# Performance work log

Hardware: AMD Instinct MI355X
Metric: run time of the kernel (lower is better)

The kernel has to match this reference:

```python
import jax, jax.numpy as jnp
import numpy as np

N_NODES = 100000
EPS = 1e-12  # F.normalize eps


def _glorot(key, shape):
    fan_in, fan_out = shape[0], shape[1]
    lim = (6.0 / (fan_in + fan_out)) ** 0.5
    return jax.random.uniform(key, shape, jnp.float32, -lim, lim)


def setup_inputs() -> dict:
    key = jax.random.key(0)
    ks = jax.random.split(key, 8)
    d_in, d_hid, d_out = 128, 128, 64
    x = jax.random.normal(ks[0], (N_NODES, d_in), jnp.float32)
    edge_index = jax.random.randint(ks[1], (2, 1600000), 0, N_NODES, jnp.int32)
    return {
        "x": x,
        "edge_index": edge_index,
        "Wl1": _glorot(ks[2], (d_in, d_hid)),
        "Wr1": _glorot(ks[3], (d_in, d_hid)),
        "b1": jnp.zeros((d_hid,), jnp.float32),
        "Wl2": _glorot(ks[4], (d_hid, d_out)),
        "Wr2": _glorot(ks[5], (d_hid, d_out)),
        "b2": jnp.zeros((d_out,), jnp.float32),
    }


def _sage_conv(x, src, dst, Wl, Wr, b):
    # gather source-node features per edge, max-aggregate onto destinations
    msgs = x[src]                                   # [E, d]
    agg = jax.ops.segment_max(msgs, dst, num_segments=N_NODES)
    # PyG scatter-max leaves 0 for nodes with no incoming edges
    agg = jnp.where(jnp.isneginf(agg), 0.0, agg)    # [N, d]
    out = agg @ Wl + x @ Wr + b                     # lin_l(aggr) + lin_r(root)
    # normalize=True -> L2 normalize rows (F.normalize semantics)
    norm = jnp.maximum(jnp.linalg.norm(out, axis=-1, keepdims=True), EPS)
    return out / norm


def reference(x, edge_index, Wl1, Wr1, b1, Wl2, Wr2, b2):
    src, dst = edge_index[0], edge_index[1]
    # dropout p=0.9 is identity in eval mode
    h = jax.nn.relu(_sage_conv(x, src, dst, Wl1, Wr1, b1))
    return _sage_conv(h, src, dst, Wl2, Wr2, b2)
```

## Files before the change

### kernel.cpp

```cpp
#include <hip/hip_runtime.h>
#include <math.h>

typedef __attribute__((ext_vector_type(8))) short short8;
typedef __attribute__((ext_vector_type(4))) float floatx4;

static __device__ __forceinline__ ushort f32_to_bf16_rne(float f) {
  union { float f; unsigned int i; } c;
  c.f = f;
  unsigned int lsb = (c.i >> 16) & 1u;
  c.i += 0x7fffu + lsb;
  return (ushort)(c.i >> 16);
}
static __device__ __forceinline__ float bf16_lo(unsigned int v) {
  union { unsigned int i; float f; } c;
  c.i = v << 16;
  return c.f;
}
static __device__ __forceinline__ float bf16_hi(unsigned int v) {
  union { unsigned int i; float f; } c;
  c.i = v & 0xffff0000u;
  return c.f;
}


#define NBLK 256

__global__ __launch_bounds__(256) void binhist_kernel(const int* __restrict__ dst,
                                                      int* __restrict__ bh, int E, int EBLK,
                                                      int NBUCKET) {
  __shared__ int h[256];
  int t = threadIdx.x, blk = blockIdx.x;
  h[t] = 0;
  __syncthreads();
  int e0 = blk * EBLK, e1 = min(E, e0 + EBLK);
  for (int e = e0 + t; e < e1; e += 256) atomicAdd(&h[dst[e] >> 9], 1);
  __syncthreads();
  if (t < NBUCKET) bh[t * NBLK + blk] = h[t];
}

__global__ void scan1_kernel(const int* __restrict__ counts, int* __restrict__ offsets,
                             int* __restrict__ tileSums, int N) {
  __shared__ int sd[256];
  int t = threadIdx.x;
  int base = blockIdx.x * 1024 + t * 4;
  int v[4];
#pragma unroll
  for (int i = 0; i < 4; i++) v[i] = (base + i < N) ? counts[base + i] : 0;
  int s = v[0] + v[1] + v[2] + v[3];
  sd[t] = s;
  __syncthreads();
  int acc = s;
  for (int off = 1; off < 256; off <<= 1) {
    int add = (t >= off) ? sd[t - off] : 0;
    __syncthreads();
    acc += add;
    sd[t] = acc;
    __syncthreads();
  }
  int run = acc - s;
#pragma unroll
  for (int i = 0; i < 4; i++) {
    if (base + i < N) offsets[base + i] = run;
    run += v[i];
  }
  if (t == 255) tileSums[blockIdx.x] = acc;
}

__global__ void scan2_kernel(int* __restrict__ tileSums, int nT) {
  __shared__ int sd[128];
  int t = threadIdx.x;
  int v = (t < nT) ? tileSums[t] : 0;
  sd[t] = v;
  __syncthreads();
  int acc = v;
  for (int off = 1; off < 128; off <<= 1) {
    int add = (t >= off) ? sd[t - off] : 0;
    __syncthreads();
    acc += add;
    sd[t] = acc;
    __syncthreads();
  }
  if (t < nT) tileSums[t] = acc - v;
}

__global__ void scan3_nc_kernel(int* __restrict__ offsets, const int* __restrict__ tileSums,
                                int N) {
  int i = blockIdx.x * 256 + threadIdx.x;
  if (i >= N) return;
  offsets[i] += tileSums[i >> 10];
}

__global__ __launch_bounds__(256) void binscatter_kernel(const int* __restrict__ src,
                                                         const int* __restrict__ dst,
                                                         const int* __restrict__ bhOff,
                                                         int2* __restrict__ binned, int E,
                                                         int EBLK, int NBUCKET) {
  __shared__ int cur[256];
  int t = threadIdx.x, blk = blockIdx.x;
  if (t < NBUCKET) cur[t] = bhOff[t * NBLK + blk];
  __syncthreads();
  int e0 = blk * EBLK, e1 = min(E, e0 + EBLK);
  for (int e = e0 + t; e < e1; e += 256) {
    int d = dst[e];
    int pos = atomicAdd(&cur[d >> 9], 1);
    binned[pos] = make_int2(src[e], d);
  }
}

__global__ __launch_bounds__(256) void bucket_build_kernel(
    const int2* __restrict__ binned, const int* __restrict__ bhOff, int* __restrict__ counts,
    int* __restrict__ offsets, int* __restrict__ csr, int N, int E, int NBUCKET) {
  __shared__ int h[512];
  __shared__ int lofs[512];
  __shared__ int cur[512];
  __shared__ int sd[256];
  int b = blockIdx.x, t = threadIdx.x;
  int S = bhOff[b * NBLK];
  int Send = (b + 1 < NBUCKET) ? bhOff[(b + 1) * NBLK] : E;
  h[t] = 0;
  h[t + 256] = 0;
  __syncthreads();
  for (int e = S + t; e < Send; e += 256) atomicAdd(&h[binned[e].y & 511], 1);
  __syncthreads();
  int h0 = h[2 * t], h1 = h[2 * t + 1];
  int s = h0 + h1;
  sd[t] = s;
  __syncthreads();
  int acc = s;
  for (int off = 1; off < 256; off <<= 1) {
    int add = (t >= off) ? sd[t - off] : 0;
    __syncthreads();
    acc += add;
    sd[t] = acc;
    __syncthreads();
  }
  int run = acc - s;
  lofs[2 * t] = run;
  lofs[2 * t + 1] = run + h0;
  __syncthreads();
  int node0 = b * 512;
#pragma unroll
  for (int i = 0; i < 2; i++) {
    int l = t + i * 256;
    int node = node0 + l;
    if (node < N) {
      counts[node] = h[l];
      offsets[node] = S + lofs[l];
    }
    cur[l] = S + lofs[l];
  }
  __syncthreads();
  for (int e = S + t; e < Send; e += 256) {
    int2 r = binned[e];
    int pos = atomicAdd(&cur[r.y & 511], 1);
    csr[pos] = r.x;
  }
}


__global__ void f32_to_bf16_kernel(const float* __restrict__ in, ushort* __restrict__ out, int n) {
  int i = (blockIdx.x * 256 + threadIdx.x) * 8;
  if (i >= n) return;
  float4 a = *(const float4*)(in + i);
  float4 b = *(const float4*)(in + i + 4);
  union { ushort u[8]; short8 v; } r;
  r.u[0] = f32_to_bf16_rne(a.x); r.u[1] = f32_to_bf16_rne(a.y);
  r.u[2] = f32_to_bf16_rne(a.z); r.u[3] = f32_to_bf16_rne(a.w);
  r.u[4] = f32_to_bf16_rne(b.x); r.u[5] = f32_to_bf16_rne(b.y);
  r.u[6] = f32_to_bf16_rne(b.z); r.u[7] = f32_to_bf16_rne(b.w);
  *(short8*)(out + i) = r.v;
}

__global__ void wt_conv_kernel(const float* __restrict__ W, ushort* __restrict__ WT, int K, int C) {
  int idx = blockIdx.x * 256 + threadIdx.x;
  if (idx >= K * C) return;
  int k = idx / C, c = idx % C;
  WT[(size_t)c * K + k] = f32_to_bf16_rne(W[idx]);
}


__global__ void agg_max_bf16_kernel(const ushort* __restrict__ feat, const int* __restrict__ csr,
                                    const int* __restrict__ offsets, const int* __restrict__ counts,
                                    unsigned int* __restrict__ aggb, int N) {
  int lane = threadIdx.x & 63;
  int node = (blockIdx.x * blockDim.x + threadIdx.x) >> 6;
  if (node >= N) return;
  const unsigned int* fu = (const unsigned int*)feat;
  int start = offsets[node];
  int deg = counts[node];
  float m0 = 0.0f, m1 = 0.0f;
  if (deg > 0) {
    m0 = -INFINITY;
    m1 = -INFINITY;
    int e = 0;
    for (; e + 4 <= deg; e += 4) {
      int s0 = csr[start + e + 0];
      int s1 = csr[start + e + 1];
      int s2 = csr[start + e + 2];
      int s3 = csr[start + e + 3];
      unsigned int v0 = fu[(size_t)s0 * 64 + lane];
      unsigned int v1 = fu[(size_t)s1 * 64 + lane];
      unsigned int v2 = fu[(size_t)s2 * 64 + lane];
      unsigned int v3 = fu[(size_t)s3 * 64 + lane];
      m0 = fmaxf(m0, fmaxf(fmaxf(bf16_lo(v0), bf16_lo(v1)), fmaxf(bf16_lo(v2), bf16_lo(v3))));
      m1 = fmaxf(m1, fmaxf(fmaxf(bf16_hi(v0), bf16_hi(v1)), fmaxf(bf16_hi(v2), bf16_hi(v3))));
    }
    for (; e < deg; e++) {
      unsigned int v = fu[(size_t)csr[start + e] * 64 + lane];
      m0 = fmaxf(m0, bf16_lo(v));
      m1 = fmaxf(m1, bf16_hi(v));
    }
  }
  unsigned int res = (__float_as_uint(m0) >> 16) | (__float_as_uint(m1) & 0xffff0000u);
  aggb[(size_t)node * 64 + lane] = res;
}


template <int DOUT, bool RELU, bool OUTBF16>
__global__ __launch_bounds__(256) void gemm_mfma_kernel(
    const ushort* __restrict__ A, const ushort* __restrict__ X, const ushort* __restrict__ WlT,
    const ushort* __restrict__ WrT, const float* __restrict__ bias, void* __restrict__ outp,
    int N) {
  constexpr int D = 128;
  constexpr int NCT = DOUT / 16;
  int t = threadIdx.x;
  int lane = t & 63;
  int wid = t >> 6;
  int l16 = lane & 15;
  int lk = lane >> 4;
  int rowbase = blockIdx.x * 128 + wid * 32;

  floatx4 acc[2][NCT];
#pragma unroll
  for (int rt = 0; rt < 2; rt++)
#pragma unroll
    for (int ct = 0; ct < NCT; ct++) acc[rt][ct] = (floatx4){0.f, 0.f, 0.f, 0.f};

  int ra = rowbase + l16;       if (ra > N - 1) ra = N - 1;
  int rb = rowbase + 16 + l16;  if (rb > N - 1) rb = N - 1;
  const ushort* pA0 = A + (size_t)ra * D;
  const ushort* pA1 = A + (size_t)rb * D;
  const ushort* pX0 = X + (size_t)ra * D;
  const ushort* pX1 = X + (size_t)rb * D;

#pragma unroll
  for (int kc = 0; kc < 4; kc++) {
    int ko = kc * 32 + lk * 8;
    short8 a0 = *(const short8*)(pA0 + ko);
    short8 a1 = *(const short8*)(pA1 + ko);
    short8 x0 = *(const short8*)(pX0 + ko);
    short8 x1 = *(const short8*)(pX1 + ko);
#pragma unroll
    for (int ct = 0; ct < NCT; ct++) {
      int c = ct * 16 + l16;
      short8 bl = *(const short8*)(WlT + (size_t)c * D + ko);
      short8 br = *(const short8*)(WrT + (size_t)c * D + ko);
      acc[0][ct] = __builtin_amdgcn_mfma_f32_16x16x32_bf16(a0, bl, acc[0][ct], 0, 0, 0);
      acc[0][ct] = __builtin_amdgcn_mfma_f32_16x16x32_bf16(x0, br, acc[0][ct], 0, 0, 0);
      acc[1][ct] = __builtin_amdgcn_mfma_f32_16x16x32_bf16(a1, bl, acc[1][ct], 0, 0, 0);
      acc[1][ct] = __builtin_amdgcn_mfma_f32_16x16x32_bf16(x1, br, acc[1][ct], 0, 0, 0);
    }
  }

  float bb[NCT];
#pragma unroll
  for (int ct = 0; ct < NCT; ct++) bb[ct] = bias[ct * 16 + l16];
#pragma unroll
  for (int rt = 0; rt < 2; rt++)
#pragma unroll
    for (int ct = 0; ct < NCT; ct++)
#pragma unroll
      for (int r = 0; r < 4; r++) acc[rt][ct][r] += bb[ct];

#pragma unroll
  for (int rt = 0; rt < 2; rt++) {
#pragma unroll
    for (int r = 0; r < 4; r++) {
      float ss = 0.f;
#pragma unroll
      for (int ct = 0; ct < NCT; ct++) ss += acc[rt][ct][r] * acc[rt][ct][r];
      ss += __shfl_xor(ss, 1);
      ss += __shfl_xor(ss, 2);
      ss += __shfl_xor(ss, 4);
      ss += __shfl_xor(ss, 8);
      float inv = 1.0f / fmaxf(sqrtf(ss), 1e-12f);
      int n = rowbase + rt * 16 + lk * 4 + r;
      if (n < N) {
#pragma unroll
        for (int ct = 0; ct < NCT; ct++) {
          float v = acc[rt][ct][r] * inv;
          if (RELU) v = fmaxf(v, 0.f);
          size_t o = (size_t)n * DOUT + ct * 16 + l16;
          if (OUTBF16)
            ((ushort*)outp)[o] = f32_to_bf16_rne(v);
          else
            ((float*)outp)[o] = v;
        }
      }
    }
  }
}


extern "C" void kernel_launch(void* const* d_in, const int* in_sizes, int n_in, void* d_out,
                              int out_size, void* d_ws, size_t ws_size, hipStream_t stream) {
  const float* x = (const float*)d_in[0];
  const int* ei = (const int*)d_in[1];
  const float* Wl1 = (const float*)d_in[2];
  const float* Wr1 = (const float*)d_in[3];
  const float* b1 = (const float*)d_in[4];
  const float* Wl2 = (const float*)d_in[5];
  const float* Wr2 = (const float*)d_in[6];
  const float* b2 = (const float*)d_in[7];
  float* out = (float*)d_out;

  const int E = in_sizes[1] / 2;
  const int N = in_sizes[0] / 128;
  const int D = 128;

  const int* src = ei;
  const int* dst = ei + E;

  char* w = (char*)d_ws;
  size_t off = 0;
  auto alloc = [&](size_t bytes) {
    void* p = w + off;
    off = (off + bytes + 511) & ~((size_t)511);
    return p;
  };
  const int NBUCKET = (N + 511) >> 9;
  const int M = NBUCKET * NBLK;
  int* bh = (int*)alloc((size_t)M * 4);
  int* tileSums = (int*)alloc(512);
  int* counts = (int*)alloc((size_t)N * 4);
  int* offsets = (int*)alloc((size_t)N * 4);
  int2* binned = (int2*)alloc((size_t)E * 8);
  int* csr = (int*)alloc((size_t)E * 4);
  ushort* xb = (ushort*)alloc((size_t)N * D * 2);
  ushort* aggb = (ushort*)alloc((size_t)N * D * 2);
  ushort* hb = (ushort*)alloc((size_t)N * D * 2);
  ushort* WlT1 = (ushort*)alloc(128 * 128 * 2);
  ushort* WrT1 = (ushort*)alloc(128 * 128 * 2);
  ushort* WlT2 = (ushort*)alloc(128 * 64 * 2);
  ushort* WrT2 = (ushort*)alloc(128 * 64 * 2);
  (void)ws_size;

  const int EBLK = (E + NBLK - 1) / NBLK;
  const int nTiles = (M + 1023) / 1024;

  binhist_kernel<<<NBLK, 256, 0, stream>>>(dst, bh, E, EBLK, NBUCKET);
  scan1_kernel<<<nTiles, 256, 0, stream>>>(bh, bh, tileSums, M);
  scan2_kernel<<<1, 128, 0, stream>>>(tileSums, nTiles);
  scan3_nc_kernel<<<(M + 255) / 256, 256, 0, stream>>>(bh, tileSums, M);
  binscatter_kernel<<<NBLK, 256, 0, stream>>>(src, dst, bh, binned, E, EBLK, NBUCKET);
  bucket_build_kernel<<<NBUCKET, 256, 0, stream>>>(binned, bh, counts, offsets, csr, N, E,
                                                   NBUCKET);

  f32_to_bf16_kernel<<<(N * D / 8 + 255) / 256, 256, 0, stream>>>(x, xb, N * D);
  wt_conv_kernel<<<(128 * 128 + 255) / 256, 256, 0, stream>>>(Wl1, WlT1, 128, 128);
  wt_conv_kernel<<<(128 * 128 + 255) / 256, 256, 0, stream>>>(Wr1, WrT1, 128, 128);
  wt_conv_kernel<<<(128 * 64 + 255) / 256, 256, 0, stream>>>(Wl2, WlT2, 128, 64);
  wt_conv_kernel<<<(128 * 64 + 255) / 256, 256, 0, stream>>>(Wr2, WrT2, 128, 64);

  const int nbGemm = (N + 127) / 128;

  agg_max_bf16_kernel<<<(N * 64 + 255) / 256, 256, 0, stream>>>(xb, csr, offsets, counts,
                                                                (unsigned int*)aggb, N);
  gemm_mfma_kernel<128, true, true>
      <<<nbGemm, 256, 0, stream>>>(aggb, xb, WlT1, WrT1, b1, hb, N);

  agg_max_bf16_kernel<<<(N * 64 + 255) / 256, 256, 0, stream>>>(hb, csr, offsets, counts,
                                                                (unsigned int*)aggb, N);
  gemm_mfma_kernel<64, false, false>
      <<<nbGemm, 256, 0, stream>>>(aggb, hb, WlT2, WrT2, b2, out, N);
}
```

Before: 396.7 us.

## Pack binned edges into 32-bit words, fuse weight conversions, unroll aggregation

Binned edge records shrink from an int2 to one 32-bit word: the local destination index (9 bits) is packed above a 17-bit source index. This halves the scratch traffic in binscatter and bucket_build. Nontemporal loads are used for the edge streams, the four weight-transpose launches are merged into one kernel, and the max-aggregation loop is unrolled to 8 gathers with a wave-uniform node index. The packing assumes source ids fit in 17 bits, which holds for N=100000 but breaks for larger graphs.

```diff
diff --git a/kernel.cpp b/kernel.cpp
--- a/kernel.cpp
+++ b/kernel.cpp
@@ -33,7 +33,7 @@
   h[t] = 0;
   __syncthreads();
   int e0 = blk * EBLK, e1 = min(E, e0 + EBLK);
-  for (int e = e0 + t; e < e1; e += 256) atomicAdd(&h[dst[e] >> 9], 1);
+  for (int e = e0 + t; e < e1; e += 256) atomicAdd(&h[__builtin_nontemporal_load(dst + e) >> 9], 1);
   __syncthreads();
   if (t < NBUCKET) bh[t * NBLK + blk] = h[t];
 }
@@ -93,7 +93,7 @@
 __global__ __launch_bounds__(256) void binscatter_kernel(const int* __restrict__ src,
                                                          const int* __restrict__ dst,
                                                          const int* __restrict__ bhOff,
-                                                         int2* __restrict__ binned, int E,
+                                                         unsigned int* __restrict__ binned, int E,
                                                          int EBLK, int NBUCKET) {
   __shared__ int cur[256];
   int t = threadIdx.x, blk = blockIdx.x;
@@ -101,15 +101,17 @@
   __syncthreads();
   int e0 = blk * EBLK, e1 = min(E, e0 + EBLK);
   for (int e = e0 + t; e < e1; e += 256) {
-    int d = dst[e];
+    int d = __builtin_nontemporal_load(dst + e);
+    int s = __builtin_nontemporal_load(src + e);
     int pos = atomicAdd(&cur[d >> 9], 1);
-    binned[pos] = make_int2(src[e], d);
+    binned[pos] = ((unsigned int)(d & 511) << 17) | (unsigned int)s;
   }
 }
 
 __global__ __launch_bounds__(256) void bucket_build_kernel(
-    const int2* __restrict__ binned, const int* __restrict__ bhOff, int* __restrict__ counts,
-    int* __restrict__ offsets, int* __restrict__ csr, int N, int E, int NBUCKET) {
+    const unsigned int* __restrict__ binned, const int* __restrict__ bhOff,
+    int* __restrict__ counts, int* __restrict__ offsets, int* __restrict__ csr, int N, int E,
+    int NBUCKET) {
   __shared__ int h[512];
   __shared__ int lofs[512];
   __shared__ int cur[512];
@@ -120,7 +122,10 @@
   h[t] = 0;
   h[t + 256] = 0;
   __syncthreads();
-  for (int e = S + t; e < Send; e += 256) atomicAdd(&h[binned[e].y & 511], 1);
+  for (int e = S + t; e < Send; e += 256) {
+    unsigned int rv = __builtin_nontemporal_load(binned + e);
+    atomicAdd(&h[(rv >> 17) & 511], 1);
+  }
   __syncthreads();
   int h0 = h[2 * t], h1 = h[2 * t + 1];
   int s = h0 + h1;
@@ -151,9 +156,9 @@
   }
   __syncthreads();
   for (int e = S + t; e < Send; e += 256) {
-    int2 r = binned[e];
-    int pos = atomicAdd(&cur[r.y & 511], 1);
-    csr[pos] = r.x;
+    unsigned int rv = __builtin_nontemporal_load(binned + e);
+    int pos = atomicAdd(&cur[(rv >> 17) & 511], 1);
+    csr[pos] = (int)(rv & 0x1ffffu);
   }
 }
 
@@ -171,19 +176,29 @@
   *(short8*)(out + i) = r.v;
 }
 
-__global__ void wt_conv_kernel(const float* __restrict__ W, ushort* __restrict__ WT, int K, int C) {
+__global__ void wt_conv_all_kernel(const float* __restrict__ Wl1, const float* __restrict__ Wr1,
+                                   const float* __restrict__ Wl2, const float* __restrict__ Wr2,
+                                   ushort* __restrict__ WlT1, ushort* __restrict__ WrT1,
+                                   ushort* __restrict__ WlT2, ushort* __restrict__ WrT2) {
   int idx = blockIdx.x * 256 + threadIdx.x;
-  if (idx >= K * C) return;
-  int k = idx / C, c = idx % C;
-  WT[(size_t)c * K + k] = f32_to_bf16_rne(W[idx]);
-}
-
-
-__global__ void agg_max_bf16_kernel(const ushort* __restrict__ feat, const int* __restrict__ csr,
-                                    const int* __restrict__ offsets, const int* __restrict__ counts,
-                                    unsigned int* __restrict__ aggb, int N) {
+  const float* W;
+  ushort* WT;
+  int C, base;
+  if (idx < 16384)      { W = Wl1; WT = WlT1; C = 128; base = idx; }
+  else if (idx < 32768) { W = Wr1; WT = WrT1; C = 128; base = idx - 16384; }
+  else if (idx < 40960) { W = Wl2; WT = WlT2; C = 64;  base = idx - 32768; }
+  else                  { W = Wr2; WT = WrT2; C = 64;  base = idx - 40960; }
+  int k = base / C, c = base % C;
+  WT[c * 128 + k] = f32_to_bf16_rne(W[base]);
+}
+
+
+__global__ __launch_bounds__(256) void agg_max_bf16_kernel(
+    const ushort* __restrict__ feat, const int* __restrict__ csr,
+    const int* __restrict__ offsets, const int* __restrict__ counts,
+    unsigned int* __restrict__ aggb, int N) {
   int lane = threadIdx.x & 63;
-  int node = (blockIdx.x * blockDim.x + threadIdx.x) >> 6;
+  int node = __builtin_amdgcn_readfirstlane((int)((blockIdx.x * 256 + threadIdx.x) >> 6));
   if (node >= N) return;
   const unsigned int* fu = (const unsigned int*)feat;
   int start = offsets[node];
@@ -192,21 +207,26 @@
   if (deg > 0) {
     m0 = -INFINITY;
     m1 = -INFINITY;
+    const int* ce = csr + start;
     int e = 0;
-    for (; e + 4 <= deg; e += 4) {
-      int s0 = csr[start + e + 0];
-      int s1 = csr[start + e + 1];
-      int s2 = csr[start + e + 2];
-      int s3 = csr[start + e + 3];
+    for (; e + 8 <= deg; e += 8) {
+      int s0 = ce[e + 0], s1 = ce[e + 1], s2 = ce[e + 2], s3 = ce[e + 3];
+      int s4 = ce[e + 4], s5 = ce[e + 5], s6 = ce[e + 6], s7 = ce[e + 7];
       unsigned int v0 = fu[(size_t)s0 * 64 + lane];
       unsigned int v1 = fu[(size_t)s1 * 64 + lane];
       unsigned int v2 = fu[(size_t)s2 * 64 + lane];
       unsigned int v3 = fu[(size_t)s3 * 64 + lane];
+      unsigned int v4 = fu[(size_t)s4 * 64 + lane];
+      unsigned int v5 = fu[(size_t)s5 * 64 + lane];
+      unsigned int v6 = fu[(size_t)s6 * 64 + lane];
+      unsigned int v7 = fu[(size_t)s7 * 64 + lane];
       m0 = fmaxf(m0, fmaxf(fmaxf(bf16_lo(v0), bf16_lo(v1)), fmaxf(bf16_lo(v2), bf16_lo(v3))));
+      m0 = fmaxf(m0, fmaxf(fmaxf(bf16_lo(v4), bf16_lo(v5)), fmaxf(bf16_lo(v6), bf16_lo(v7))));
       m1 = fmaxf(m1, fmaxf(fmaxf(bf16_hi(v0), bf16_hi(v1)), fmaxf(bf16_hi(v2), bf16_hi(v3))));
+      m1 = fmaxf(m1, fmaxf(fmaxf(bf16_hi(v4), bf16_hi(v5)), fmaxf(bf16_hi(v6), bf16_hi(v7))));
     }
     for (; e < deg; e++) {
-      unsigned int v = fu[(size_t)csr[start + e] * 64 + lane];
+      unsigned int v = fu[(size_t)ce[e] * 64 + lane];
       m0 = fmaxf(m0, bf16_lo(v));
       m1 = fmaxf(m1, bf16_hi(v));
     }
@@ -334,7 +354,7 @@
   int* tileSums = (int*)alloc(512);
   int* counts = (int*)alloc((size_t)N * 4);
   int* offsets = (int*)alloc((size_t)N * 4);
-  int2* binned = (int2*)alloc((size_t)E * 8);
+  unsigned int* binned = (unsigned int*)alloc((size_t)E * 4);
   int* csr = (int*)alloc((size_t)E * 4);
   ushort* xb = (ushort*)alloc((size_t)N * D * 2);
   ushort* aggb = (ushort*)alloc((size_t)N * D * 2);
@@ -357,10 +377,7 @@
                                                    NBUCKET);
 
   f32_to_bf16_kernel<<<(N * D / 8 + 255) / 256, 256, 0, stream>>>(x, xb, N * D);
-  wt_conv_kernel<<<(128 * 128 + 255) / 256, 256, 0, stream>>>(Wl1, WlT1, 128, 128);
-  wt_conv_kernel<<<(128 * 128 + 255) / 256, 256, 0, stream>>>(Wr1, WrT1, 128, 128);
-  wt_conv_kernel<<<(128 * 64 + 255) / 256, 256, 0, stream>>>(Wl2, WlT2, 128, 64);
-  wt_conv_kernel<<<(128 * 64 + 255) / 256, 256, 0, stream>>>(Wr2, WrT2, 128, 64);
+  wt_conv_all_kernel<<<192, 256, 0, stream>>>(Wl1, Wr1, Wl2, Wr2, WlT1, WrT1, WlT2, WrT2);
 
   const int nbGemm = (N + 127) / 128;
 
```

Result: faster. 361.5 us (-8.9%).
